# Kernel optimization log

Hardware: AMD Instinct MI355X
Metric: run time of the kernel (lower is better)

## Reference

```python
import jax, jax.numpy as jnp
import numpy as np

N = 100_000      # nodes
E = 3_200_000    # edges
B = 1024         # graphs in batch
IN = 4           # in_channels
G = 16           # GCNNodes
D = 32           # NDenseNodes


def _linear_params(k, out_f, in_f):
    s = 1.0 / np.sqrt(in_f)
    kw, kb = jax.random.split(k)
    W = jax.random.uniform(kw, (out_f, in_f), jnp.float32, -s, s)
    b = jax.random.uniform(kb, (out_f,), jnp.float32, -s, s)
    return W, b


def setup_inputs() -> dict:
    key = jax.random.key(0)
    ks = jax.random.split(key, 12)
    X = jax.random.normal(ks[0], (N, IN), jnp.float32)
    Edge_index = jax.random.randint(ks[1], (2, E), 0, N, jnp.int64)
    Edge_weight = jax.random.uniform(ks[2], (E,), jnp.float32)
    Batching = jnp.sort(jax.random.randint(ks[3], (N,), 0, B, jnp.int64))
    W1, b1 = _linear_params(ks[4], G, IN)   # Conv1 lin (PyG GCNConv: Linear no bias + bias param)
    W2, b2 = _linear_params(ks[5], G, G)    # Conv2
    C1w, C1b = _linear_params(ks[6], D, 2 * G)
    C2w, C2b = _linear_params(ks[7], D, D)
    C3w, C3b = _linear_params(ks[8], 1, D)
    R1w, R1b = _linear_params(ks[9], D, 2 * G)
    R2w, R2b = _linear_params(ks[10], D, D)
    R3w, R3b = _linear_params(ks[11], 1, D)
    return {"X": X, "Edge_index": Edge_index, "Edge_weight": Edge_weight,
            "Batching": Batching, "num_graphs": B,
            "W1": W1, "b1": b1, "W2": W2, "b2": b2,
            "C1w": C1w, "C1b": C1b, "C2w": C2w, "C2b": C2b, "C3w": C3w, "C3b": C3b,
            "R1w": R1w, "R1b": R1b, "R2w": R2w, "R2b": R2b, "R3w": R3w, "R3b": R3b}


def _gcn_conv(x, row, col, w, W, b):
    """PyG GCNConv: add self loops (weight 1), symmetric norm, x@W.T, scatter-add at col, +b."""
    n = x.shape[0]
    loop = jnp.arange(n)
    row2 = jnp.concatenate([row, loop])
    col2 = jnp.concatenate([col, loop])
    w2 = jnp.concatenate([w, jnp.ones((n,), x.dtype)])
    deg = jax.ops.segment_sum(w2, col2, num_segments=n)          # deg >= 1 via self loops
    dinv = jnp.where(deg > 0, jax.lax.rsqrt(deg), 0.0)
    norm = dinv[row2] * w2 * dinv[col2]                           # [E+n]
    xw = x @ W.T                                                  # [n, out]
    out = jax.ops.segment_sum(norm[:, None] * xw[row2], col2, num_segments=n)
    return out + b


def reference(X, Edge_index, Edge_weight, Batching, num_graphs,
              W1, b1, W2, b2, C1w, C1b, C2w, C2b, C3w, C3b,
              R1w, R1b, R2w, R2b, R3w, R3b):
    act = jax.nn.leaky_relu  # default slope 0.01, matches nn.LeakyReLU()
    row, col = Edge_index[0], Edge_index[1]
    # add_self_loops then keep only col > row  ==  zero out weights where col <= row
    w = jnp.where(col > row, Edge_weight, 0.0)

    out = act(_gcn_conv(X, row, col, w, W1, b1))
    out = act(_gcn_conv(out, row, col, w, W2, b2))

    ones = jnp.ones((out.shape[0],), out.dtype)
    cnt = jax.ops.segment_sum(ones, Batching, num_segments=num_graphs)
    outMean = jax.ops.segment_sum(out, Batching, num_segments=num_graphs) / jnp.maximum(cnt, 1.0)[:, None]
    outMax = jax.ops.segment_max(out, Batching, num_segments=num_graphs)
    pooled = jnp.concatenate([outMean, outMax], axis=1)           # [B, 2G]

    Chi0 = act(pooled @ C1w.T + C1b)
    Chi0 = act(Chi0 @ C2w.T + C2b)
    Chi0 = Chi0 @ C3w.T + C3b
    Rp = act(pooled @ R1w.T + R1b)
    Rp = act(Rp @ R2w.T + R2b)
    Rp = Rp @ R3w.T + R3b
    return jnp.concatenate([Chi0, Rp], axis=1)                    # [B, 2]
```

## Files before the change

kernel.cpp:

```cpp
#include <hip/hip_runtime.h>
#include <hip/hip_bf16.h>
#include <float.h>

#define LRELU(x) ((x) > 0.0f ? (x) : 0.01f * (x))

typedef unsigned int u32;
typedef unsigned long long u64;

#define WSUM_MASK  ((1u << 25) - 1)
#define CNT_ONE    (1u << 25)

__device__ __forceinline__ float dinv_of(u32 d) {
    return rsqrtf(1.0f + (float)(d & WSUM_MASK) * (1.0f / 131072.0f));
}


__global__ __launch_bounds__(256) void k_countb(const int* __restrict__ row,
                                                const int* __restrict__ col,
                                                const float* __restrict__ w,
                                                const float* __restrict__ X,
                                                const float* __restrict__ W1,
                                                u32* __restrict__ deg32,
                                                u32* __restrict__ pack,
                                                float* __restrict__ xw1,
                                                int E, int N, int gE, int cap) {
    int tid = threadIdx.x;
    if ((int)blockIdx.x < gE) {
        int e = blockIdx.x * 256 + tid;
        if (e >= E) return;
        int r = row[e], c = col[e];
        if (c <= r) return;
        float wv = w[e];
        u32 q15 = (u32)(wv * 32768.0f);
        if (q15 > 32767u) q15 = 32767u;
        u32 old = atomicAdd(deg32 + c, CNT_ONE | (u32)(wv * 131072.0f));
        u32 rank = old >> 25;
        if (rank < (u32)cap)
            pack[(size_t)c * cap + rank] = ((u32)r << 15) | q15;
    } else {
        int i = (blockIdx.x - gE) * 256 + tid;
        if (i >= N) return;
        const float4 x = *reinterpret_cast<const float4*>(X + 4 * i);
        float o[16];
#pragma unroll
        for (int g = 0; g < 16; ++g) {
            const float4 wr = *reinterpret_cast<const float4*>(W1 + 4 * g);
            o[g] = x.x * wr.x + x.y * wr.y + x.z * wr.z + x.w * wr.w;
        }
        float4* dst = reinterpret_cast<float4*>(xw1 + 16 * i);
#pragma unroll
        for (int k = 0; k < 4; ++k)
            dst[k] = make_float4(o[4 * k], o[4 * k + 1], o[4 * k + 2], o[4 * k + 3]);
    }
}

__global__ __launch_bounds__(256) void k_gather1b(const u32* __restrict__ deg32,
                                                  const u32* __restrict__ pack,
                                                  const float* __restrict__ xw1,
                                                  const float* __restrict__ b1,
                                                  const float* __restrict__ W2,
                                                  float* __restrict__ xs2,
                                                  int N, int cap) {
    int t = blockIdx.x * blockDim.x + threadIdx.x;
    int NT = 16 * N;
    bool valid = t < NT;
    int tc = valid ? t : NT - 1;
    int c = tc >> 4, g = tc & 15;
    u32 dc_raw = deg32[c];
    int cnt = (int)(dc_raw >> 25);
    if (cnt > cap) cnt = cap;
    float dc = dinv_of(dc_raw);
    float s = dc * xw1[tc];
    const uint4* bp = reinterpret_cast<const uint4*>(pack + (size_t)c * cap);
    int nv = (cnt + 3) >> 2;
    for (int q = 0; q < nv; ++q) {
        uint4 pv = bp[q];
        int bj = q << 2;
#pragma unroll
        for (int k = 0; k < 4; ++k) {
            u32 p = (k == 0) ? pv.x : (k == 1) ? pv.y : (k == 2) ? pv.z : pv.w;
            if (bj + k < cnt) {
                u32 r = p >> 15;
                float dr = dinv_of(deg32[r]);
                s += (float)(p & 32767u) * (1.0f / 32768.0f) * dr *
                     xw1[((size_t)r << 4) + g];
            }
        }
    }
    float h = dc * s + b1[g];
    h = LRELU(h);
    int lane = threadIdx.x & 63;
    int base = lane & 48;
    const float4* W2r = reinterpret_cast<const float4*>(W2 + 16 * g);
    float4 w0 = W2r[0], w1 = W2r[1], w2 = W2r[2], w3 = W2r[3];
    float o = 0.0f;
    o += __shfl(h, base + 0) * w0.x;
    o += __shfl(h, base + 1) * w0.y;
    o += __shfl(h, base + 2) * w0.z;
    o += __shfl(h, base + 3) * w0.w;
    o += __shfl(h, base + 4) * w1.x;
    o += __shfl(h, base + 5) * w1.y;
    o += __shfl(h, base + 6) * w1.z;
    o += __shfl(h, base + 7) * w1.w;
    o += __shfl(h, base + 8) * w2.x;
    o += __shfl(h, base + 9) * w2.y;
    o += __shfl(h, base + 10) * w2.z;
    o += __shfl(h, base + 11) * w2.w;
    o += __shfl(h, base + 12) * w3.x;
    o += __shfl(h, base + 13) * w3.y;
    o += __shfl(h, base + 14) * w3.z;
    o += __shfl(h, base + 15) * w3.w;
    if (valid) xs2[t] = dc * o;
}

__global__ __launch_bounds__(256) void k_gather2b(const u32* __restrict__ deg32,
                                                  const u32* __restrict__ pack,
                                                  const float* __restrict__ xs2,
                                                  const float* __restrict__ b2,
                                                  float* __restrict__ acc,
                                                  int N, int cap) {
    int t = blockIdx.x * blockDim.x + threadIdx.x;
    if (t >= 16 * N) return;
    int c = t >> 4, g = t & 15;
    u32 dc_raw = deg32[c];
    int cnt = (int)(dc_raw >> 25);
    if (cnt > cap) cnt = cap;
    float dc = dinv_of(dc_raw);
    float s = xs2[t];
    const uint4* bp = reinterpret_cast<const uint4*>(pack + (size_t)c * cap);
    int nv = (cnt + 3) >> 2;
    for (int q = 0; q < nv; ++q) {
        uint4 pv = bp[q];
        int bj = q << 2;
#pragma unroll
        for (int k = 0; k < 4; ++k) {
            u32 p = (k == 0) ? pv.x : (k == 1) ? pv.y : (k == 2) ? pv.z : pv.w;
            if (bj + k < cnt)
                s += (float)(p & 32767u) * (1.0f / 32768.0f) *
                     xs2[(((size_t)(p >> 15)) << 4) + g];
        }
    }
    float a = dc * s + b2[g];
    acc[t] = LRELU(a);
}

__global__ __launch_bounds__(64) void k_poolA(const float* __restrict__ acc,
                                              const int* __restrict__ batching,
                                              int N,
                                              const float* __restrict__ C1w, const float* __restrict__ C1b,
                                              const float* __restrict__ C2w, const float* __restrict__ C2b,
                                              const float* __restrict__ C3w, const float* __restrict__ C3b,
                                              const float* __restrict__ R1w, const float* __restrict__ R1b,
                                              const float* __restrict__ R2w, const float* __restrict__ R2b,
                                              const float* __restrict__ R3w, const float* __restrict__ R3b,
                                              float* __restrict__ out) {
    int b = blockIdx.x;
    int t = threadIdx.x;
    __shared__ int s_se[2];
    __shared__ float sp[32];
    __shared__ float h1s[64];
    __shared__ float h2s[64];
    if (t < 2) {
        int target = b + t;
        int lo = 0, hi = N;
        while (lo < hi) {
            int mid = (lo + hi) >> 1;
            if (batching[mid] < target) lo = mid + 1; else hi = mid;
        }
        s_se[t] = lo;
    }
    __syncthreads();
    int start = s_se[0], end = s_se[1];
    int g = t & 15, sub = t >> 4;
    float sum = 0.0f, mx = -FLT_MAX;
    for (int n = start + sub; n < end; n += 4) {
        float v = acc[16 * n + g];
        sum += v;
        mx = fmaxf(mx, v);
    }
    sum += __shfl_down(sum, 32);
    mx = fmaxf(mx, __shfl_down(mx, 32));
    sum += __shfl_down(sum, 16);
    mx = fmaxf(mx, __shfl_down(mx, 16));
    if (t < 16) {
        float cnt = (float)(end - start);
        sp[t] = sum / fmaxf(cnt, 1.0f);
        sp[16 + t] = mx;
    }
    __syncthreads();
    int d = t & 31;
    const float* W1h = (t < 32) ? C1w : R1w;
    const float* b1h = (t < 32) ? C1b : R1b;
    float a1 = b1h[d];
#pragma unroll 4
    for (int k = 0; k < 32; ++k) a1 += sp[k] * W1h[32 * d + k];
    h1s[t] = LRELU(a1);
    __syncthreads();
    const float* W2h = (t < 32) ? C2w : R2w;
    const float* b2h = (t < 32) ? C2b : R2b;
    const float* h1base = h1s + (t < 32 ? 0 : 32);
    float a2 = b2h[d];
#pragma unroll 4
    for (int k = 0; k < 32; ++k) a2 += h1base[k] * W2h[32 * d + k];
    h2s[t] = LRELU(a2);
    __syncthreads();
    if (t == 0 || t == 32) {
        const float* w3 = (t == 0) ? C3w : R3w;
        float a3 = (t == 0) ? C3b[0] : R3b[0];
        const float* hb = h2s + t;
#pragma unroll 4
        for (int k = 0; k < 32; ++k) a3 += hb[k] * w3[k];
        out[2 * b + (t >> 5)] = a3;
    }
}

__global__ __launch_bounds__(256) void k_initf(const float* __restrict__ X,
                                               const float* __restrict__ W1,
                                               float* __restrict__ deg,
                                               float* __restrict__ xw, int N) {
    int i = blockIdx.x * blockDim.x + threadIdx.x;
    if (i >= N) return;
    deg[i] = 1.0f;
    const float4 x = *reinterpret_cast<const float4*>(X + 4 * i);
    float o[16];
#pragma unroll
    for (int g = 0; g < 16; ++g) {
        const float4 wr = *reinterpret_cast<const float4*>(W1 + 4 * g);
        o[g] = x.x * wr.x + x.y * wr.y + x.z * wr.z + x.w * wr.w;
    }
    float4* dst = reinterpret_cast<float4*>(xw + 16 * i);
#pragma unroll
    for (int k = 0; k < 4; ++k)
        dst[k] = make_float4(o[4 * k], o[4 * k + 1], o[4 * k + 2], o[4 * k + 3]);
}

__global__ __launch_bounds__(256) void k_degf(const int* __restrict__ row,
                                              const int* __restrict__ col,
                                              const float* __restrict__ w,
                                              float* __restrict__ deg, int E) {
    int e = blockIdx.x * blockDim.x + threadIdx.x;
    if (e >= E) return;
    int r = row[e], c = col[e];
    if (c > r) atomicAdd(deg + c, w[e]);
}

__global__ __launch_bounds__(256) void k_self(float* __restrict__ deg_dinv,
                                              const float* __restrict__ xw,
                                              float* __restrict__ acc, int N) {
    int i = blockIdx.x * blockDim.x + threadIdx.x;
    if (i >= N) return;
    float d = rsqrtf(deg_dinv[i]);
    deg_dinv[i] = d;
    float s = d * d;
    const float4* xs = reinterpret_cast<const float4*>(xw + 16 * i);
    float4* as = reinterpret_cast<float4*>(acc + 16 * i);
#pragma unroll
    for (int k = 0; k < 4; ++k) {
        float4 v = xs[k];
        as[k] = make_float4(s * v.x, s * v.y, s * v.z, s * v.w);
    }
}

__global__ __launch_bounds__(256) void k_scatter(const int* __restrict__ row,
                                                 const int* __restrict__ col,
                                                 const float* __restrict__ w,
                                                 const float* __restrict__ dinv,
                                                 const float* __restrict__ xw,
                                                 float* __restrict__ acc, int E) {
    int e = blockIdx.x * blockDim.x + threadIdx.x;
    if (e >= E) return;
    int r = row[e], c = col[e];
    if (c <= r) return;
    float nrm = dinv[r] * w[e] * dinv[c];
    const float4* xr = reinterpret_cast<const float4*>(xw + 16 * r);
    float* ac = acc + 16 * c;
#pragma unroll
    for (int k = 0; k < 4; ++k) {
        float4 v = xr[k];
        atomicAdd(ac + 4 * k + 0, nrm * v.x);
        atomicAdd(ac + 4 * k + 1, nrm * v.y);
        atomicAdd(ac + 4 * k + 2, nrm * v.z);
        atomicAdd(ac + 4 * k + 3, nrm * v.w);
    }
}

__global__ __launch_bounds__(256) void k_mid(const float* __restrict__ b1,
                                             const float* __restrict__ W2,
                                             const float* __restrict__ dinv,
                                             float* __restrict__ xw,
                                             float* __restrict__ acc, int N) {
    int i = blockIdx.x * blockDim.x + threadIdx.x;
    if (i >= N) return;
    float h[16];
#pragma unroll
    for (int g = 0; g < 16; ++g) {
        float v = acc[16 * i + g] + b1[g];
        h[g] = LRELU(v);
    }
    float d = dinv[i];
    float s = d * d;
#pragma unroll
    for (int g = 0; g < 16; ++g) {
        float a = 0.0f;
#pragma unroll
        for (int k = 0; k < 16; ++k) a += h[k] * W2[16 * g + k];
        xw[16 * i + g] = a;
        acc[16 * i + g] = s * a;
    }
}

__global__ __launch_bounds__(256) void k_act(const float* __restrict__ b2,
                                             float* __restrict__ acc, int NT) {
    int t = blockIdx.x * blockDim.x + threadIdx.x;
    if (t >= NT) return;
    float v = acc[t] + b2[t & 15];
    acc[t] = LRELU(v);
}

extern "C" void kernel_launch(void* const* d_in, const int* in_sizes, int n_in,
                              void* d_out, int out_size, void* d_ws, size_t ws_size,
                              hipStream_t stream) {
    const float* X   = (const float*)d_in[0];
    const int*   EI  = (const int*)d_in[1];
    const float* EW  = (const float*)d_in[2];
    const int*   Bat = (const int*)d_in[3];
    const float* W1  = (const float*)d_in[5];
    const float* b1  = (const float*)d_in[6];
    const float* W2  = (const float*)d_in[7];
    const float* b2  = (const float*)d_in[8];
    const float* C1w = (const float*)d_in[9];
    const float* C1b = (const float*)d_in[10];
    const float* C2w = (const float*)d_in[11];
    const float* C2b = (const float*)d_in[12];
    const float* C3w = (const float*)d_in[13];
    const float* C3b = (const float*)d_in[14];
    const float* R1w = (const float*)d_in[15];
    const float* R1b = (const float*)d_in[16];
    const float* R2w = (const float*)d_in[17];
    const float* R2b = (const float*)d_in[18];
    const float* R3w = (const float*)d_in[19];
    const float* R3b = (const float*)d_in[20];

    const int N = in_sizes[0] / 4;
    const int E = in_sizes[1] / 2;
    const int B = out_size / 2;
    const int* row = EI;
    const int* col = EI + E;

    float* outp = (float*)d_out;

    dim3 blk(256);
    const int gN  = (N + 255) / 256;
    const int gE  = (E + 255) / 256;
    const int gNG = (16 * N + 255) / 256;

    int cap = 0;
    {
        size_t base = (size_t)N * (1 + 16 + 16) + 8;
        if ((base + (size_t)96 * N) * 4 <= ws_size) cap = 96;
        else if ((base + (size_t)80 * N) * 4 <= ws_size) cap = 80;
    }

    if (cap > 0) {
        size_t off = 0;
        u32*   deg32 = (u32*)d_ws;          off += (size_t)N;
        float* xs1   = (float*)d_ws + off;  off += 16 * (size_t)N;
        float* xs2   = (float*)d_ws + off;  off += 16 * (size_t)N;
        off = (off + 3) & ~(size_t)3;
        u32*   pack  = (u32*)d_ws + off;
        float* acc   = xs1;

        hipMemsetAsync(deg32, 0, (size_t)N * sizeof(u32), stream);
        k_countb<<<dim3(gE + gN), blk, 0, stream>>>(row, col, EW, X, W1,
                                                    deg32, pack, xs1, E, N, gE, cap);
        k_gather1b<<<dim3(gNG), blk, 0, stream>>>(deg32, pack, xs1, b1, W2,
                                                  xs2, N, cap);
        k_gather2b<<<dim3(gNG), blk, 0, stream>>>(deg32, pack, xs2, b2,
                                                  acc, N, cap);
        k_poolA <<<dim3(B), dim3(64), 0, stream>>>(acc, Bat, N,
                                                   C1w, C1b, C2w, C2b, C3w, C3b,
                                                   R1w, R1b, R2w, R2b, R3w, R3b,
                                                   outp);
        return;
    }

    float* deg = (float*)d_ws;
    float* xw  = (float*)d_ws + N;
    float* acc = xw + 16 * (size_t)N;
    k_initf<<<dim3(gN), blk, 0, stream>>>(X, W1, deg, xw, N);
    k_degf <<<dim3(gE), blk, 0, stream>>>(row, col, EW, deg, E);
    k_self <<<dim3(gN), blk, 0, stream>>>(deg, xw, acc, N);
    k_scatter<<<dim3(gE), blk, 0, stream>>>(row, col, EW, deg, xw, acc, E);
    k_mid  <<<dim3(gN), blk, 0, stream>>>(b1, W2, deg, xw, acc, N);
    k_scatter<<<dim3(gE), blk, 0, stream>>>(row, col, EW, deg, xw, acc, E);
    k_act  <<<dim3(gNG), blk, 0, stream>>>(b2, acc, 16 * N);
    k_poolA<<<dim3(B), dim3(64), 0, stream>>>(acc, Bat, N,
                                              C1w, C1b, C2w, C2b, C3w, C3b,
                                              R1w, R1b, R2w, R2b, R3w, R3b,
                                              outp);
}
```

Baseline: 220.7 us.

## Fuse second GCN gather with graph pooling and prescale features by dinv

Adds a prep kernel that computes dinv once per node and prescales the layer-1 features by it, so the first gather no longer does a random deg32 lookup and rsqrt per neighbour. The second gather is fused into the pooling/MLP kernel, with one 256-thread block per graph, which drops the acc write and read plus one launch. The packed adjacency stores become nontemporal. The fused kernel has only B=1024 blocks, with 16 nodes in flight per block, so the gather may lose parallelism and latency hiding compared with the old full-grid launch.

Result: slower. 280.7 us (+27.2%).

```diff
diff --git a/kernel.cpp b/kernel.cpp
--- a/kernel.cpp
+++ b/kernel.cpp
@@ -36,7 +36,8 @@
         u32 old = atomicAdd(deg32 + c, CNT_ONE | (u32)(wv * 131072.0f));
         u32 rank = old >> 25;
         if (rank < (u32)cap)
-            pack[(size_t)c * cap + rank] = ((u32)r << 15) | q15;
+            __builtin_nontemporal_store(((u32)r << 15) | q15,
+                                        pack + (size_t)c * cap + rank);
     } else {
         int i = (blockIdx.x - gE) * 256 + tid;
         if (i >= N) return;
@@ -54,9 +55,25 @@
     }
 }
 
+__global__ __launch_bounds__(256) void k_prep(const u32* __restrict__ deg32,
+                                              float* __restrict__ dinv,
+                                              float* __restrict__ xw, int N) {
+    int i = blockIdx.x * blockDim.x + threadIdx.x;
+    if (i >= N) return;
+    float dv = dinv_of(deg32[i]);
+    dinv[i] = dv;
+    float4* p = reinterpret_cast<float4*>(xw + 16 * i);
+#pragma unroll
+    for (int q = 0; q < 4; ++q) {
+        float4 t = p[q];
+        p[q] = make_float4(dv * t.x, dv * t.y, dv * t.z, dv * t.w);
+    }
+}
+
 __global__ __launch_bounds__(256) void k_gather1b(const u32* __restrict__ deg32,
                                                   const u32* __restrict__ pack,
-                                                  const float* __restrict__ xw1,
+                                                  const float* __restrict__ xs1,
+                                                  const float* __restrict__ dinv,
                                                   const float* __restrict__ b1,
                                                   const float* __restrict__ W2,
                                                   float* __restrict__ xs2,
@@ -66,11 +83,10 @@
     bool valid = t < NT;
     int tc = valid ? t : NT - 1;
     int c = tc >> 4, g = tc & 15;
-    u32 dc_raw = deg32[c];
-    int cnt = (int)(dc_raw >> 25);
+    int cnt = (int)(deg32[c] >> 25);
     if (cnt > cap) cnt = cap;
-    float dc = dinv_of(dc_raw);
-    float s = dc * xw1[tc];
+    float dc = dinv[c];
+    float s = xs1[tc];
     const uint4* bp = reinterpret_cast<const uint4*>(pack + (size_t)c * cap);
     int nv = (cnt + 3) >> 2;
     for (int q = 0; q < nv; ++q) {
@@ -79,12 +95,9 @@
 #pragma unroll
         for (int k = 0; k < 4; ++k) {
             u32 p = (k == 0) ? pv.x : (k == 1) ? pv.y : (k == 2) ? pv.z : pv.w;
-            if (bj + k < cnt) {
-                u32 r = p >> 15;
-                float dr = dinv_of(deg32[r]);
-                s += (float)(p & 32767u) * (1.0f / 32768.0f) * dr *
-                     xw1[((size_t)r << 4) + g];
-            }
+            if (bj + k < cnt)
+                s += (float)(p & 32767u) * (1.0f / 32768.0f) *
+                     xs1[(((size_t)(p >> 15)) << 4) + g];
         }
     }
     float h = dc * s + b1[g];
@@ -113,35 +126,211 @@
     if (valid) xs2[t] = dc * o;
 }
 
-__global__ __launch_bounds__(256) void k_gather2b(const u32* __restrict__ deg32,
-                                                  const u32* __restrict__ pack,
-                                                  const float* __restrict__ xs2,
-                                                  const float* __restrict__ b2,
-                                                  float* __restrict__ acc,
-                                                  int N, int cap) {
+__global__ __launch_bounds__(256) void k_g2pool(const u32* __restrict__ deg32,
+                                                const u32* __restrict__ pack,
+                                                const float* __restrict__ xs2,
+                                                const float* __restrict__ b2,
+                                                const int* __restrict__ batching,
+                                                int N, int cap,
+                                                const float* __restrict__ C1w, const float* __restrict__ C1b,
+                                                const float* __restrict__ C2w, const float* __restrict__ C2b,
+                                                const float* __restrict__ C3w, const float* __restrict__ C3b,
+                                                const float* __restrict__ R1w, const float* __restrict__ R1b,
+                                                const float* __restrict__ R2w, const float* __restrict__ R2b,
+                                                const float* __restrict__ R3w, const float* __restrict__ R3b,
+                                                float* __restrict__ out) {
+    int b = blockIdx.x;
+    int t = threadIdx.x;
+    __shared__ int s_se[2];
+    __shared__ float ssum[256], smax[256];
+    __shared__ float sp[32];
+    __shared__ float h1s[64], h2s[64];
+    if (t < 2) {
+        int target = b + t;
+        int lo = 0, hi = N;
+        while (lo < hi) {
+            int mid = (lo + hi) >> 1;
+            if (batching[mid] < target) lo = mid + 1; else hi = mid;
+        }
+        s_se[t] = lo;
+    }
+    __syncthreads();
+    int start = s_se[0], end = s_se[1];
+    int g = t & 15, sub = t >> 4;
+    float bg = b2[g];
+    float sum = 0.0f, mx = -FLT_MAX;
+    for (int n = start + sub; n < end; n += 16) {
+        u32 draw = deg32[n];
+        int cnt = (int)(draw >> 25);
+        if (cnt > cap) cnt = cap;
+        float dc = dinv_of(draw);
+        float s = xs2[16 * (size_t)n + g];
+        const uint4* bp = reinterpret_cast<const uint4*>(pack + (size_t)n * cap);
+        int nv = (cnt + 3) >> 2;
+        for (int q = 0; q < nv; ++q) {
+            uint4 pv = bp[q];
+            int bj = q << 2;
+#pragma unroll
+            for (int k = 0; k < 4; ++k) {
+                u32 p = (k == 0) ? pv.x : (k == 1) ? pv.y : (k == 2) ? pv.z : pv.w;
+                if (bj + k < cnt)
+                    s += (float)(p & 32767u) * (1.0f / 32768.0f) *
+                         xs2[(((size_t)(p >> 15)) << 4) + g];
+            }
+        }
+        float v = dc * s + bg;
+        v = LRELU(v);
+        sum += v;
+        mx = fmaxf(mx, v);
+    }
+    ssum[t] = sum; smax[t] = mx;
+    __syncthreads();
+#pragma unroll
+    for (int off = 128; off >= 16; off >>= 1) {
+        if (t < off) {
+            ssum[t] += ssum[t + off];
+            smax[t] = fmaxf(smax[t], smax[t + off]);
+        }
+        __syncthreads();
+    }
+    if (t < 16) {
+        float cntf = (float)(end - start);
+        sp[t] = ssum[t] / fmaxf(cntf, 1.0f);
+        sp[16 + t] = smax[t];
+    }
+    __syncthreads();
+    if (t < 64) {
+        int d = t & 31;
+        const float* W1h = (t < 32) ? C1w : R1w;
+        const float* b1h = (t < 32) ? C1b : R1b;
+        float a1 = b1h[d];
+#pragma unroll 4
+        for (int k = 0; k < 32; ++k) a1 += sp[k] * W1h[32 * d + k];
+        h1s[t] = LRELU(a1);
+    }
+    __syncthreads();
+    if (t < 64) {
+        int d = t & 31;
+        const float* W2h = (t < 32) ? C2w : R2w;
+        const float* b2h = (t < 32) ? C2b : R2b;
+        const float* h1base = h1s + (t < 32 ? 0 : 32);
+        float a2 = b2h[d];
+#pragma unroll 4
+        for (int k = 0; k < 32; ++k) a2 += h1base[k] * W2h[32 * d + k];
+        h2s[t] = LRELU(a2);
+    }
+    __syncthreads();
+    if (t == 0 || t == 32) {
+        const float* w3 = (t == 0) ? C3w : R3w;
+        float a3 = (t == 0) ? C3b[0] : R3b[0];
+        const float* hb = h2s + t;
+#pragma unroll 4
+        for (int k = 0; k < 32; ++k) a3 += hb[k] * w3[k];
+        out[2 * b + (t >> 5)] = a3;
+    }
+}
+
+__global__ __launch_bounds__(256) void k_initf(const float* __restrict__ X,
+                                               const float* __restrict__ W1,
+                                               float* __restrict__ deg,
+                                               float* __restrict__ xw, int N) {
+    int i = blockIdx.x * blockDim.x + threadIdx.x;
+    if (i >= N) return;
+    deg[i] = 1.0f;
+    const float4 x = *reinterpret_cast<const float4*>(X + 4 * i);
+    float o[16];
+#pragma unroll
+    for (int g = 0; g < 16; ++g) {
+        const float4 wr = *reinterpret_cast<const float4*>(W1 + 4 * g);
+        o[g] = x.x * wr.x + x.y * wr.y + x.z * wr.z + x.w * wr.w;
+    }
+    float4* dst = reinterpret_cast<float4*>(xw + 16 * i);
+#pragma unroll
+    for (int k = 0; k < 4; ++k)
+        dst[k] = make_float4(o[4 * k], o[4 * k + 1], o[4 * k + 2], o[4 * k + 3]);
+}
+
+__global__ __launch_bounds__(256) void k_degf(const int* __restrict__ row,
+                                              const int* __restrict__ col,
+                                              const float* __restrict__ w,
+                                              float* __restrict__ deg, int E) {
+    int e = blockIdx.x * blockDim.x + threadIdx.x;
+    if (e >= E) return;
+    int r = row[e], c = col[e];
+    if (c > r) atomicAdd(deg + c, w[e]);
+}
+
+__global__ __launch_bounds__(256) void k_self(float* __restrict__ deg_dinv,
+                                              const float* __restrict__ xw,
+                                              float* __restrict__ acc, int N) {
+    int i = blockIdx.x * blockDim.x + threadIdx.x;
+    if (i >= N) return;
+    float d = rsqrtf(deg_dinv[i]);
+    deg_dinv[i] = d;
+    float s = d * d;
+    const float4* xs = reinterpret_cast<const float4*>(xw + 16 * i);
+    float4* as = reinterpret_cast<float4*>(acc + 16 * i);
+#pragma unroll
+    for (int k = 0; k < 4; ++k) {
+        float4 v = xs[k];
+        as[k] = make_float4(s * v.x, s * v.y, s * v.z, s * v.w);
+    }
+}
+
+__global__ __launch_bounds__(256) void k_scatter(const int* __restrict__ row,
+                                                 const int* __restrict__ col,
+                                                 const float* __restrict__ w,
+                                                 const float* __restrict__ dinv,
+                                                 const float* __restrict__ xw,
+                                                 float* __restrict__ acc, int E) {
+    int e = blockIdx.x * blockDim.x + threadIdx.x;
+    if (e >= E) return;
+    int r = row[e], c = col[e];
+    if (c <= r) return;
+    float nrm = dinv[r] * w[e] * dinv[c];
+    const float4* xr = reinterpret_cast<const float4*>(xw + 16 * r);
+    float* ac = acc + 16 * c;
+#pragma unroll
+    for (int k = 0; k < 4; ++k) {
+        float4 v = xr[k];
+        atomicAdd(ac + 4 * k + 0, nrm * v.x);
+        atomicAdd(ac + 4 * k + 1, nrm * v.y);
+        atomicAdd(ac + 4 * k + 2, nrm * v.z);
+        atomicAdd(ac + 4 * k + 3, nrm * v.w);
+    }
+}
+
+__global__ __launch_bounds__(256) void k_mid(const float* __restrict__ b1,
+                                             const float* __restrict__ W2,
+                                             const float* __restrict__ dinv,
+                                             float* __restrict__ xw,
+                                             float* __restrict__ acc, int N) {
+    int i = blockIdx.x * blockDim.x + threadIdx.x;
+    if (i >= N) return;
+    float h[16];
+#pragma unroll
+    for (int g = 0; g < 16; ++g) {
+        float v = acc[16 * i + g] + b1[g];
+        h[g] = LRELU(v);
+    }
+    float d = dinv[i];
+    float s = d * d;
+#pragma unroll
+    for (int g = 0; g < 16; ++g) {
+        float a = 0.0f;
+#pragma unroll
+        for (int k = 0; k < 16; ++k) a += h[k] * W2[16 * g + k];
+        xw[16 * i + g] = a;
+        acc[16 * i + g] = s * a;
+    }
+}
+
+__global__ __launch_bounds__(256) void k_act(const float* __restrict__ b2,
+                                             float* __restrict__ acc, int NT) {
     int t = blockIdx.x * blockDim.x + threadIdx.x;
-    if (t >= 16 * N) return;
-    int c = t >> 4, g = t & 15;
-    u32 dc_raw = deg32[c];
-    int cnt = (int)(dc_raw >> 25);
-    if (cnt > cap) cnt = cap;
-    float dc = dinv_of(dc_raw);
-    float s = xs2[t];
-    const uint4* bp = reinterpret_cast<const uint4*>(pack + (size_t)c * cap);
-    int nv = (cnt + 3) >> 2;
-    for (int q = 0; q < nv; ++q) {
-        uint4 pv = bp[q];
-        int bj = q << 2;
-#pragma unroll
-        for (int k = 0; k < 4; ++k) {
-            u32 p = (k == 0) ? pv.x : (k == 1) ? pv.y : (k == 2) ? pv.z : pv.w;
-            if (bj + k < cnt)
-                s += (float)(p & 32767u) * (1.0f / 32768.0f) *
-                     xs2[(((size_t)(p >> 15)) << 4) + g];
-        }
-    }
-    float a = dc * s + b2[g];
-    acc[t] = LRELU(a);
+    if (t >= NT) return;
+    float v = acc[t] + b2[t & 15];
+    acc[t] = LRELU(v);
 }
 
 __global__ __launch_bounds__(64) void k_poolA(const float* __restrict__ acc,
@@ -212,109 +401,6 @@
         for (int k = 0; k < 32; ++k) a3 += hb[k] * w3[k];
         out[2 * b + (t >> 5)] = a3;
     }
-}
-
-__global__ __launch_bounds__(256) void k_initf(const float* __restrict__ X,
-                                               const float* __restrict__ W1,
-                                               float* __restrict__ deg,
-                                               float* __restrict__ xw, int N) {
-    int i = blockIdx.x * blockDim.x + threadIdx.x;
-    if (i >= N) return;
-    deg[i] = 1.0f;
-    const float4 x = *reinterpret_cast<const float4*>(X + 4 * i);
-    float o[16];
-#pragma unroll
-    for (int g = 0; g < 16; ++g) {
-        const float4 wr = *reinterpret_cast<const float4*>(W1 + 4 * g);
-        o[g] = x.x * wr.x + x.y * wr.y + x.z * wr.z + x.w * wr.w;
-    }
-    float4* dst = reinterpret_cast<float4*>(xw + 16 * i);
-#pragma unroll
-    for (int k = 0; k < 4; ++k)
-        dst[k] = make_float4(o[4 * k], o[4 * k + 1], o[4 * k + 2], o[4 * k + 3]);
-}
-
-__global__ __launch_bounds__(256) void k_degf(const int* __restrict__ row,
-                                              const int* __restrict__ col,
-                                              const float* __restrict__ w,
-                                              float* __restrict__ deg, int E) {
-    int e = blockIdx.x * blockDim.x + threadIdx.x;
-    if (e >= E) return;
-    int r = row[e], c = col[e];
-    if (c > r) atomicAdd(deg + c, w[e]);
-}
-
-__global__ __launch_bounds__(256) void k_self(float* __restrict__ deg_dinv,
-                                              const float* __restrict__ xw,
-                                              float* __restrict__ acc, int N) {
-    int i = blockIdx.x * blockDim.x + threadIdx.x;
-    if (i >= N) return;
-    float d = rsqrtf(deg_dinv[i]);
-    deg_dinv[i] = d;
-    float s = d * d;
-    const float4* xs = reinterpret_cast<const float4*>(xw + 16 * i);
-    float4* as = reinterpret_cast<float4*>(acc + 16 * i);
-#pragma unroll
-    for (int k = 0; k < 4; ++k) {
-        float4 v = xs[k];
-        as[k] = make_float4(s * v.x, s * v.y, s * v.z, s * v.w);
-    }
-}
-
-__global__ __launch_bounds__(256) void k_scatter(const int* __restrict__ row,
-                                                 const int* __restrict__ col,
-                                                 const float* __restrict__ w,
-                                                 const float* __restrict__ dinv,
-                                                 const float* __restrict__ xw,
-                                                 float* __restrict__ acc, int E) {
-    int e = blockIdx.x * blockDim.x + threadIdx.x;
-    if (e >= E) return;
-    int r = row[e], c = col[e];
-    if (c <= r) return;
-    float nrm = dinv[r] * w[e] * dinv[c];
-    const float4* xr = reinterpret_cast<const float4*>(xw + 16 * r);
-    float* ac = acc + 16 * c;
-#pragma unroll
-    for (int k = 0; k < 4; ++k) {
-        float4 v = xr[k];
-        atomicAdd(ac + 4 * k + 0, nrm * v.x);
-        atomicAdd(ac + 4 * k + 1, nrm * v.y);
-        atomicAdd(ac + 4 * k + 2, nrm * v.z);
-        atomicAdd(ac + 4 * k + 3, nrm * v.w);
-    }
-}
-
-__global__ __launch_bounds__(256) void k_mid(const float* __restrict__ b1,
-                                             const float* __restrict__ W2,
-                                             const float* __restrict__ dinv,
-                                             float* __restrict__ xw,
-                                             float* __restrict__ acc, int N) {
-    int i = blockIdx.x * blockDim.x + threadIdx.x;
-    if (i >= N) return;
-    float h[16];
-#pragma unroll
-    for (int g = 0; g < 16; ++g) {
-        float v = acc[16 * i + g] + b1[g];
-        h[g] = LRELU(v);
-    }
-    float d = dinv[i];
-    float s = d * d;
-#pragma unroll
-    for (int g = 0; g < 16; ++g) {
-        float a = 0.0f;
-#pragma unroll
-        for (int k = 0; k < 16; ++k) a += h[k] * W2[16 * g + k];
-        xw[16 * i + g] = a;
-        acc[16 * i + g] = s * a;
-    }
-}
-
-__global__ __launch_bounds__(256) void k_act(const float* __restrict__ b2,
-                                             float* __restrict__ acc, int NT) {
-    int t = blockIdx.x * blockDim.x + threadIdx.x;
-    if (t >= NT) return;
-    float v = acc[t] + b2[t & 15];
-    acc[t] = LRELU(v);
 }
 
 extern "C" void kernel_launch(void* const* d_in, const int* in_sizes, int n_in,
@@ -356,7 +442,7 @@
 
     int cap = 0;
     {
-        size_t base = (size_t)N * (1 + 16 + 16) + 8;
+        size_t base = (size_t)N * (1 + 16 + 16 + 1) + 8;
         if ((base + (size_t)96 * N) * 4 <= ws_size) cap = 96;
         else if ((base + (size_t)80 * N) * 4 <= ws_size) cap = 80;
     }
@@ -366,21 +452,20 @@
         u32*   deg32 = (u32*)d_ws;          off += (size_t)N;
         float* xs1   = (float*)d_ws + off;  off += 16 * (size_t)N;
         float* xs2   = (float*)d_ws + off;  off += 16 * (size_t)N;
+        float* dinv  = (float*)d_ws + off;  off += (size_t)N;
         off = (off + 3) & ~(size_t)3;
         u32*   pack  = (u32*)d_ws + off;
-        float* acc   = xs1;
 
         hipMemsetAsync(deg32, 0, (size_t)N * sizeof(u32), stream);
         k_countb<<<dim3(gE + gN), blk, 0, stream>>>(row, col, EW, X, W1,
                                                     deg32, pack, xs1, E, N, gE, cap);
-        k_gather1b<<<dim3(gNG), blk, 0, stream>>>(deg32, pack, xs1, b1, W2,
+        k_prep  <<<dim3(gN), blk, 0, stream>>>(deg32, dinv, xs1, N);
+        k_gather1b<<<dim3(gNG), blk, 0, stream>>>(deg32, pack, xs1, dinv, b1, W2,
                                                   xs2, N, cap);
-        k_gather2b<<<dim3(gNG), blk, 0, stream>>>(deg32, pack, xs2, b2,
-                                                  acc, N, cap);
-        k_poolA <<<dim3(B), dim3(64), 0, stream>>>(acc, Bat, N,
-                                                   C1w, C1b, C2w, C2b, C3w, C3b,
-                                                   R1w, R1b, R2w, R2b, R3w, R3b,
-                                                   outp);
+        k_g2pool<<<dim3(B), blk, 0, stream>>>(deg32, pack, xs2, b2, Bat, N, cap,
+                                              C1w, C1b, C2w, C2b, C3w, C3b,
+                                              R1w, R1b, R2w, R2b, R3w, R3b,
+                                              outp);
         return;
     }
 
```
